# Optimization experiments

Hardware: AMD Instinct MI355X
Metric: run time of the kernel (lower is better)

## Reference

```python
import jax, jax.numpy as jnp
import numpy as np
import math

H, NH, NKV, HD, FF = 1024, 16, 4, 64, 4096
B, S = 2, 2048
EPS, THETA = 1e-6, 10000.0


def _rmsnorm(x, w, eps=EPS):
    v = jnp.mean(x.astype(jnp.float32) ** 2, axis=-1, keepdims=True)
    return (x.astype(jnp.float32) * jax.lax.rsqrt(v + eps)).astype(x.dtype) * w


def _rope_tables(seq_len, head_dim, theta=THETA):
    inv_freq = 1.0 / (theta ** (jnp.arange(0, head_dim, 2, dtype=jnp.float32) / head_dim))
    freqs = jnp.arange(seq_len, dtype=jnp.float32)[:, None] * inv_freq[None, :]
    emb = jnp.concatenate([freqs, freqs], axis=-1)  # [S, HD]
    return jnp.cos(emb), jnp.sin(emb)


def _rotate_half(x):
    x1, x2 = jnp.split(x, 2, axis=-1)
    return jnp.concatenate([-x2, x1], axis=-1)


def _apply_rope(x, cos, sin):
    # x: [B, h, S, HD]; cos/sin: [S, HD] broadcast over batch/heads
    return x * cos[None, None] + _rotate_half(x) * sin[None, None]


def setup_inputs() -> dict:
    key = jax.random.key(0)
    ks = jax.random.split(key, 12)
    std = 0.02
    return {
        "hidden_states": jax.random.normal(ks[0], (B, S, H), jnp.float32),
        "kv_states": jax.random.normal(ks[1], (B, S, H), jnp.float32),
        "attention_mask": jnp.zeros((B, 1, S, S), jnp.float32),
        "ln1_w": jnp.ones((H,), jnp.float32),
        "ln2_w": jnp.ones((H,), jnp.float32),
        "Wq": jax.random.normal(ks[2], (H, NH * HD), jnp.float32) * std,
        "Wk": jax.random.normal(ks[3], (H, NKV * HD), jnp.float32) * std,
        "Wv": jax.random.normal(ks[4], (H, NKV * HD), jnp.float32) * std,
        "Wo": jax.random.normal(ks[5], (NH * HD, H), jnp.float32) * std,
        "Wgate": jax.random.normal(ks[6], (H, FF), jnp.float32) * std,
        "Wup": jax.random.normal(ks[7], (H, FF), jnp.float32) * std,
        "Wdown": jax.random.normal(ks[8], (FF, H), jnp.float32) * std,
    }


def reference(hidden_states, kv_states, attention_mask, ln1_w, ln2_w,
              Wq, Wk, Wv, Wo, Wgate, Wup, Wdown):
    bsz, q_len, _ = hidden_states.shape
    k_len = kv_states.shape[1]

    residual = hidden_states
    h = _rmsnorm(hidden_states, ln1_w)   # input_layernorm on queries
    kv = _rmsnorm(kv_states, ln1_w)      # same norm applied to kv_states

    q = (h @ Wq).reshape(bsz, q_len, NH, HD).transpose(0, 2, 1, 3)    # [B,NH,Sq,HD]
    k = (kv @ Wk).reshape(bsz, k_len, NKV, HD).transpose(0, 2, 1, 3)  # [B,NKV,Sk,HD]
    v = (kv @ Wv).reshape(bsz, k_len, NKV, HD).transpose(0, 2, 1, 3)

    cos_q, sin_q = _rope_tables(q_len, HD)
    cos_k, sin_k = _rope_tables(k_len, HD)
    q = _apply_rope(q, cos_q, sin_q)
    k = _apply_rope(k, cos_k, sin_k)

    # repeat_kv: GQA expand to NH heads
    groups = NH // NKV
    k = jnp.repeat(k, groups, axis=1)
    v = jnp.repeat(v, groups, axis=1)

    scores = jnp.einsum("bhqd,bhkd->bhqk", q, k) / math.sqrt(HD)
    scores = scores + attention_mask  # additive mask [B,1,Sq,Sk]
    probs = jax.nn.softmax(scores.astype(jnp.float32), axis=-1).astype(q.dtype)
    attn = jnp.einsum("bhqk,bhkd->bhqd", probs, v)
    attn = attn.transpose(0, 2, 1, 3).reshape(bsz, q_len, NH * HD)
    attn = attn @ Wo

    hidden = residual + attn

    residual = hidden
    x = _rmsnorm(hidden, ln2_w)
    x = (jax.nn.silu(x @ Wgate) * (x @ Wup)) @ Wdown  # SwiGLU MLP
    return residual + x
```

## Files before the change

kernel.cpp:

```cpp
#include <hip/hip_runtime.h>
#include <math.h>

#define SS 2048

typedef __attribute__((ext_vector_type(8))) short s16x8;
typedef __attribute__((ext_vector_type(4))) float f32x4;
typedef __attribute__((ext_vector_type(16))) float f32x16;

__device__ __forceinline__ unsigned short f2bf(float f) {
  union { float f; unsigned u; } a; a.f = f;
  unsigned r = a.u + 0x7fffu + ((a.u >> 16) & 1u);
  return (unsigned short)(r >> 16);
}
__device__ __forceinline__ float bf2f(unsigned short b) {
  union { unsigned u; float f; } a; a.u = ((unsigned)b) << 16;
  return a.f;
}
__device__ __forceinline__ unsigned cvtpk(float a, float b) {
  unsigned d; asm("v_cvt_pk_bf16_f32 %0, %1, %2" : "=v"(d) : "v"(a), "v"(b)); return d;
}
__device__ __forceinline__ float fexp2(float x) {
  float r; asm("v_exp_f32 %0, %1" : "=v"(r) : "v"(x)); return r;
}
__device__ __forceinline__ void async16(void* lds, const void* g) {
  __builtin_amdgcn_global_load_lds(
      (const __attribute__((address_space(1))) unsigned int*)g,
      (__attribute__((address_space(3))) unsigned int*)lds, 16, 0, 0);
}
__device__ __forceinline__ f32x4 mfma_bf16(s16x8 a, s16x8 b, f32x4 c) {
  return __builtin_amdgcn_mfma_f32_16x16x32_bf16(a, b, c, 0, 0, 0);
}
__device__ __forceinline__ f32x16 mfma32(s16x8 a, s16x8 b, f32x16 c) {
  return __builtin_amdgcn_mfma_f32_32x32x16_bf16(a, b, c, 0, 0, 0);
}

__global__ __launch_bounds__(256) void k_transpose(const float* __restrict__ W,
                                                   unsigned short* __restrict__ WT,
                                                   int K, int N) {
  __shared__ float tile[32][33];
  int t = threadIdx.x;
  int tx = t & 31, ty = t >> 5;
  int n0 = blockIdx.x * 32, k0 = blockIdx.y * 32;
#pragma unroll
  for (int i = 0; i < 4; ++i)
    tile[ty + 8 * i][tx] = W[(size_t)(k0 + ty + 8 * i) * N + n0 + tx];
  __syncthreads();
#pragma unroll
  for (int i = 0; i < 4; ++i)
    WT[(size_t)(n0 + ty + 8 * i) * K + k0 + tx] = f2bf(tile[tx][ty + 8 * i]);
}

__global__ __launch_bounds__(256) void k_vtrans(const unsigned short* __restrict__ QKV,
                                                unsigned short* __restrict__ VT) {
  __shared__ unsigned short tile[32][33];
  int t = threadIdx.x, tx = t & 31, ty = t >> 5;
  int s0 = blockIdx.x * 32, d0 = blockIdx.y * 32;
  int bk = blockIdx.z; int b = bk >> 2, kvh = bk & 3;
#pragma unroll
  for (int i = 0; i < 4; ++i)
    tile[ty + 8 * i][tx] =
        QKV[((size_t)b * SS + s0 + ty + 8 * i) * 1536 + 1280 + kvh * 64 + d0 + tx];
  __syncthreads();
#pragma unroll
  for (int i = 0; i < 4; ++i)
    VT[((size_t)bk * 64 + d0 + ty + 8 * i) * SS + s0 + tx] = tile[tx][ty + 8 * i];
}

__global__ void k_rope_tables(float* __restrict__ cosT, float* __restrict__ sinT) {
  int idx = blockIdx.x * 256 + threadIdx.x;
  int s = idx >> 5, i = idx & 31;
  double ang = (double)s * pow(10000.0, -(double)(2 * i) / 64.0);
  cosT[idx] = (float)cos(ang);
  sinT[idx] = (float)sin(ang);
}

__global__ __launch_bounds__(256) void k_rmsnorm(const float* __restrict__ X,
                                                 const float* __restrict__ Wt,
                                                 unsigned short* __restrict__ Y) {
  int row = blockIdx.x, t = threadIdx.x;
  float4 v = ((const float4*)X)[(size_t)row * 256 + t];
  float ssq = v.x * v.x + v.y * v.y + v.z * v.z + v.w * v.w;
#pragma unroll
  for (int m = 1; m < 64; m <<= 1) ssq += __shfl_xor(ssq, m);
  __shared__ float red[4];
  if ((t & 63) == 0) red[t >> 6] = ssq;
  __syncthreads();
  float sc = rsqrtf((red[0] + red[1] + red[2] + red[3]) * (1.0f / 1024.0f) + 1e-6f);
  float4 wv = ((const float4*)Wt)[t];
  ushort4 o;
  o.x = f2bf(v.x * sc * wv.x); o.y = f2bf(v.y * sc * wv.y);
  o.z = f2bf(v.z * sc * wv.z); o.w = f2bf(v.w * sc * wv.w);
  ((ushort4*)Y)[(size_t)row * 256 + t] = o;
}

__global__ __launch_bounds__(256) void k_rope(unsigned short* __restrict__ X,
                                              const float* __restrict__ cosT,
                                              const float* __restrict__ sinT,
                                              int stride) {
  int idx = blockIdx.x * 256 + threadIdx.x;
  int seg = idx & 7, tok = idx >> 3;
  int head = blockIdx.y;
  int s = tok & (SS - 1);
  int d0 = seg * 4;
  unsigned short* p = X + (size_t)tok * stride + head * 64;
  ushort4 lo = *(ushort4*)&p[d0];
  ushort4 hi = *(ushort4*)&p[d0 + 32];
  float4 cs = *(const float4*)&cosT[s * 32 + d0];
  float4 sn = *(const float4*)&sinT[s * 32 + d0];
  ushort4 olo, ohi;
  olo.x = f2bf(bf2f(lo.x) * cs.x - bf2f(hi.x) * sn.x);
  olo.y = f2bf(bf2f(lo.y) * cs.y - bf2f(hi.y) * sn.y);
  olo.z = f2bf(bf2f(lo.z) * cs.z - bf2f(hi.z) * sn.z);
  olo.w = f2bf(bf2f(lo.w) * cs.w - bf2f(hi.w) * sn.w);
  ohi.x = f2bf(bf2f(hi.x) * cs.x + bf2f(lo.x) * sn.x);
  ohi.y = f2bf(bf2f(hi.y) * cs.y + bf2f(lo.y) * sn.y);
  ohi.z = f2bf(bf2f(hi.z) * cs.z + bf2f(lo.z) * sn.z);
  ohi.w = f2bf(bf2f(hi.w) * cs.w + bf2f(lo.w) * sn.w);
  *(ushort4*)&p[d0] = olo;
  *(ushort4*)&p[d0 + 32] = ohi;
}

template <int EPI, int BN>
__global__ __launch_bounds__(256) void k_gemm(const unsigned short* __restrict__ A,
                                              const unsigned short* __restrict__ BT,
                                              int K, int ldc,
                                              unsigned short* Cb,
                                              float* __restrict__ Cf,
                                              const float* __restrict__ Res) {
  constexpr int NW = BN / 32;
  __shared__ __align__(16) unsigned short at[128 * 32];
  __shared__ __align__(16) unsigned short bt[BN * 32];
  int t = threadIdx.x, w = t >> 6, l = t & 63;
  int g = l >> 4, c = l & 15;
  int wm = w >> 1, wn = w & 1;
  f32x4 acc[4][NW] = {};
  const unsigned short* gA = A + (size_t)(blockIdx.y * 128 + (t >> 2)) * K + (t & 3) * 8;
  const unsigned short* gB = BT + (size_t)(blockIdx.x * BN + (t >> 2)) * K + (t & 3) * 8;
  unsigned short* dA = &at[w * 512];
  unsigned short* dB = &bt[w * 512];
  const int nk = K >> 5;
  for (int kt = 0; kt < nk; ++kt) {
    async16(dA, gA);
    async16(dA + 2048, gA + (size_t)64 * K);
    async16(dB, gB);
    if (BN == 128) async16(dB + 2048, gB + (size_t)64 * K);
    gA += 32; gB += 32;
    __syncthreads();
    s16x8 af[4], bfr[NW];
#pragma unroll
    for (int m = 0; m < 4; ++m) af[m] = *(const s16x8*)&at[(wm * 64 + m * 16 + c) * 32 + g * 8];
#pragma unroll
    for (int n = 0; n < NW; ++n)
      bfr[n] = *(const s16x8*)&bt[(wn * (BN / 2) + n * 16 + c) * 32 + g * 8];
#pragma unroll
    for (int m = 0; m < 4; ++m)
#pragma unroll
      for (int n = 0; n < NW; ++n)
        acc[m][n] = mfma_bf16(af[m], bfr[n], acc[m][n]);
    __syncthreads();
  }
  size_t rb = (size_t)blockIdx.y * 128 + wm * 64;
  size_t cbase = (size_t)blockIdx.x * BN + wn * (BN / 2);
#pragma unroll
  for (int m = 0; m < 4; ++m)
#pragma unroll
    for (int n = 0; n < NW; ++n)
#pragma unroll
      for (int r = 0; r < 4; ++r) {
        size_t row = rb + m * 16 + g * 4 + r;
        size_t col = cbase + n * 16 + c;
        float v = acc[m][n][r];
        if (EPI == 0) Cb[row * ldc + col] = f2bf(v);
        else Cf[row * ldc + col] = v + Res[row * ldc + col];
      }
}

__global__ __launch_bounds__(512) void k_gateup(const unsigned short* __restrict__ A,
                                                const unsigned short* __restrict__ BTg,
                                                const unsigned short* __restrict__ BTu,
                                                unsigned short* __restrict__ Cb) {
  __shared__ __align__(16) unsigned short at[128 * 32];
  __shared__ __align__(16) unsigned short bg[128 * 32];
  __shared__ __align__(16) unsigned short bu[128 * 32];
  int t = threadIdx.x, w = t >> 6, l = t & 63;
  int g = l >> 4, c = l & 15;
  int wm = w >> 2, wn = w & 3;
  f32x4 ag[4][2] = {}, au[4][2] = {};
  const unsigned short* gA = A + (size_t)(blockIdx.y * 128 + (t >> 2)) * 1024 + (t & 3) * 8;
  const unsigned short* gG = BTg + (size_t)(blockIdx.x * 128 + (t >> 2)) * 1024 + (t & 3) * 8;
  const unsigned short* gU = BTu + (size_t)(blockIdx.x * 128 + (t >> 2)) * 1024 + (t & 3) * 8;
  unsigned short* dA = &at[w * 512];
  unsigned short* dG = &bg[w * 512];
  unsigned short* dU = &bu[w * 512];
  for (int kt = 0; kt < 32; ++kt) {
    async16(dA, gA);
    async16(dG, gG);
    async16(dU, gU);
    gA += 32; gG += 32; gU += 32;
    __syncthreads();
    s16x8 af[4], bgf[2], buf_[2];
#pragma unroll
    for (int m = 0; m < 4; ++m) af[m] = *(const s16x8*)&at[(wm * 64 + m * 16 + c) * 32 + g * 8];
#pragma unroll
    for (int n = 0; n < 2; ++n) {
      bgf[n] = *(const s16x8*)&bg[(wn * 32 + n * 16 + c) * 32 + g * 8];
      buf_[n] = *(const s16x8*)&bu[(wn * 32 + n * 16 + c) * 32 + g * 8];
    }
#pragma unroll
    for (int m = 0; m < 4; ++m)
#pragma unroll
      for (int n = 0; n < 2; ++n) {
        ag[m][n] = mfma_bf16(af[m], bgf[n], ag[m][n]);
        au[m][n] = mfma_bf16(af[m], buf_[n], au[m][n]);
      }
    __syncthreads();
  }
  size_t rb = (size_t)blockIdx.y * 128 + wm * 64;
  size_t cb = (size_t)blockIdx.x * 128 + wn * 32;
#pragma unroll
  for (int m = 0; m < 4; ++m)
#pragma unroll
    for (int n = 0; n < 2; ++n)
#pragma unroll
      for (int r = 0; r < 4; ++r) {
        size_t row = rb + m * 16 + g * 4 + r;
        size_t col = cb + n * 16 + c;
        float gv = ag[m][n][r], uv = au[m][n][r];
        Cb[row * 4096 + col] = f2bf(gv / (1.0f + __expf(-gv)) * uv);
      }
}

__global__ __launch_bounds__(256) void k_attn(const unsigned short* __restrict__ Q,
                                              const unsigned short* __restrict__ K,
                                              const unsigned short* __restrict__ VT,
                                              const float* __restrict__ mask,
                                              unsigned short* __restrict__ Out) {
  __shared__ __align__(16) unsigned short Ks[2][64 * 64];
  __shared__ __align__(16) unsigned short VTs[2][64 * 64];
  const float LOG2E = 1.44269504f;
  int t = threadIdx.x, w = t >> 6, l = t & 63;
  int q32 = l & 31, hi = l >> 5;
  int blk = blockIdx.x;
  int qt = blk & 63, kvh = (blk >> 6) & 3, b = blk >> 8;
  int head = kvh * 4 + w;
  size_t tokQ = (size_t)b * SS + qt * 32;

  s16x8 qfr[4];
#pragma unroll
  for (int d = 0; d < 4; ++d)
    qfr[d] = *(const s16x8*)&Q[(tokQ + q32) * 1536 + head * 64 + d * 16 + hi * 8];
  const s16x8 one8 = {(short)0x3F80, (short)0x3F80, (short)0x3F80, (short)0x3F80,
                      (short)0x3F80, (short)0x3F80, (short)0x3F80, (short)0x3F80};

  int id0 = t, id1 = t + 256;
  int row0 = id0 >> 3, b80 = id0 & 7;
  int row1 = id1 >> 3, b81 = id1 & 7;
  int so0 = row0 * 64 + ((b80 ^ (row0 & 7)) << 3);
  int so1 = row1 * 64 + ((b81 ^ (row1 & 7)) << 3);
  const unsigned short* gK = K + (size_t)b * SS * 1536 + kvh * 64;
  const unsigned short* gV = VT + (size_t)(b * 4 + kvh) * 64 * SS;

  int4 rK0 = *(const int4*)(gK + (size_t)row0 * 1536 + b80 * 8);
  int4 rK1 = *(const int4*)(gK + (size_t)row1 * 1536 + b81 * 8);
  int4 rV0 = *(const int4*)(gV + (size_t)row0 * SS + b80 * 8);
  int4 rV1 = *(const int4*)(gV + (size_t)row1 * SS + b81 * 8);
  *(int4*)&Ks[0][so0] = rK0; *(int4*)&Ks[0][so1] = rK1;
  *(int4*)&VTs[0][so0] = rV0; *(int4*)&VTs[0][so1] = rV1;

  const float* mrowp = mask + (size_t)b * SS * SS + (size_t)(qt * 32 + q32) * SS + 4 * hi;
  float mc0[16], mc1[16];
#pragma unroll
  for (int j = 0; j < 4; ++j) {
    float4 v0 = *(const float4*)&mrowp[8 * j];
    float4 v1 = *(const float4*)&mrowp[32 + 8 * j];
    mc0[4 * j] = v0.x; mc0[4 * j + 1] = v0.y; mc0[4 * j + 2] = v0.z; mc0[4 * j + 3] = v0.w;
    mc1[4 * j] = v1.x; mc1[4 * j + 1] = v1.y; mc1[4 * j + 2] = v1.z; mc1[4 * j + 3] = v1.w;
  }

  f32x16 aco0 = {}, aco1 = {}, acl = {};
  float mrun = -1e30f;
  __syncthreads();

  for (int kt = 0; kt < 32; ++kt) {
    const unsigned short* Kc = Ks[kt & 1];
    const unsigned short* Vc = VTs[kt & 1];
    if (kt < 31) {
      int kb = (kt + 1) * 64;
      rK0 = *(const int4*)(gK + (size_t)(kb + row0) * 1536 + b80 * 8);
      rK1 = *(const int4*)(gK + (size_t)(kb + row1) * 1536 + b81 * 8);
      rV0 = *(const int4*)(gV + (size_t)row0 * SS + kb + b80 * 8);
      rV1 = *(const int4*)(gV + (size_t)row1 * SS + kb + b81 * 8);
    }
    f32x16 s0 = {}, s1 = {};
    __builtin_amdgcn_s_setprio(1);
#pragma unroll
    for (int d = 0; d < 4; ++d) {
      s16x8 ka = *(const s16x8*)&Kc[q32 * 64 + (((d * 2 + hi) ^ (q32 & 7)) << 3)];
      s0 = mfma32(ka, qfr[d], s0);
      int r2 = 32 + q32;
      s16x8 kb2 = *(const s16x8*)&Kc[r2 * 64 + (((d * 2 + hi) ^ (r2 & 7)) << 3)];
      s1 = mfma32(kb2, qfr[d], s1);
    }
    __builtin_amdgcn_s_setprio(0);
    float sv0[16], sv1[16];
#pragma unroll
    for (int r = 0; r < 16; ++r) {
      sv0[r] = (s0[r] * 0.125f + mc0[r]) * LOG2E;
      sv1[r] = (s1[r] * 0.125f + mc1[r]) * LOG2E;
    }
    {
      int nk = (kt < 31 ? kt + 1 : 31) * 64;
#pragma unroll
      for (int j = 0; j < 4; ++j) {
        float4 v0 = *(const float4*)&mrowp[nk + 8 * j];
        float4 v1 = *(const float4*)&mrowp[nk + 32 + 8 * j];
        mc0[4 * j] = v0.x; mc0[4 * j + 1] = v0.y; mc0[4 * j + 2] = v0.z; mc0[4 * j + 3] = v0.w;
        mc1[4 * j] = v1.x; mc1[4 * j + 1] = v1.y; mc1[4 * j + 2] = v1.z; mc1[4 * j + 3] = v1.w;
      }
    }
    float mx = sv0[0];
#pragma unroll
    for (int r = 1; r < 16; ++r) mx = fmaxf(mx, sv0[r]);
#pragma unroll
    for (int r = 0; r < 16; ++r) mx = fmaxf(mx, sv1[r]);
    mx = fmaxf(mx, __shfl_xor(mx, 32));
    if (__any(mx > mrun + 8.0f)) {
      float mnew = fmaxf(mrun, mx);
      float alpha = fexp2(mrun - mnew);
      mrun = mnew;
#pragma unroll
      for (int r = 0; r < 16; ++r) {
        float al = __shfl(alpha, (r & 3) + 8 * (r >> 2) + 4 * hi);
        aco0[r] *= al; aco1[r] *= al; acl[r] *= al;
      }
    }
    s16x8 pa[4];
#pragma unroll
    for (int ks = 0; ks < 2; ++ks) {
      float p[16];
      if (ks == 0) {
#pragma unroll
        for (int r = 0; r < 16; ++r) p[r] = fexp2(sv0[r] - mrun);
      } else {
#pragma unroll
        for (int r = 0; r < 16; ++r) p[r] = fexp2(sv1[r] - mrun);
      }
      unsigned w8[8];
#pragma unroll
      for (int i = 0; i < 8; ++i) w8[i] = cvtpk(p[2 * i], p[2 * i + 1]);
      unsigned sd0 = hi ? w8[0] : w8[2];
      unsigned sd1 = hi ? w8[1] : w8[3];
      unsigned sd2 = hi ? w8[4] : w8[6];
      unsigned sd3 = hi ? w8[5] : w8[7];
      unsigned rc0 = (unsigned)__shfl_xor((int)sd0, 32);
      unsigned rc1 = (unsigned)__shfl_xor((int)sd1, 32);
      unsigned rc2 = (unsigned)__shfl_xor((int)sd2, 32);
      unsigned rc3 = (unsigned)__shfl_xor((int)sd3, 32);
      union { int4 i; s16x8 v; } fa, fb;
      fa.i.x = hi ? rc0 : w8[0]; fa.i.y = hi ? rc1 : w8[1];
      fa.i.z = hi ? w8[2] : rc0; fa.i.w = hi ? w8[3] : rc1;
      fb.i.x = hi ? rc2 : w8[4]; fb.i.y = hi ? rc3 : w8[5];
      fb.i.z = hi ? w8[6] : rc2; fb.i.w = hi ? w8[7] : rc3;
      pa[2 * ks] = fa.v;
      pa[2 * ks + 1] = fb.v;
    }
    __builtin_amdgcn_s_setprio(1);
#pragma unroll
    for (int ks = 0; ks < 4; ++ks) {
      s16x8 va = *(const s16x8*)&Vc[q32 * 64 + (((ks * 2 + hi) ^ (q32 & 7)) << 3)];
      aco0 = mfma32(pa[ks], va, aco0);
      int r2 = 32 + q32;
      s16x8 vb2 = *(const s16x8*)&Vc[r2 * 64 + (((ks * 2 + hi) ^ (r2 & 7)) << 3)];
      aco1 = mfma32(pa[ks], vb2, aco1);
      acl = mfma32(pa[ks], one8, acl);
    }
    __builtin_amdgcn_s_setprio(0);
    if (kt < 31) {
      int nb = (kt + 1) & 1;
      *(int4*)&Ks[nb][so0] = rK0; *(int4*)&Ks[nb][so1] = rK1;
      *(int4*)&VTs[nb][so0] = rV0; *(int4*)&VTs[nb][so1] = rV1;
    }
    __syncthreads();
  }
#pragma unroll
  for (int r = 0; r < 16; ++r) {
    float inv = 1.0f / acl[r];
    size_t orow = tokQ + (r & 3) + 8 * (r >> 2) + 4 * hi;
    Out[orow * 1024 + head * 64 + q32] = f2bf(aco0[r] * inv);
    Out[orow * 1024 + head * 64 + 32 + q32] = f2bf(aco1[r] * inv);
  }
}

extern "C" void kernel_launch(void* const* d_in, const int* in_sizes, int n_in,
                              void* d_out, int out_size, void* d_ws, size_t ws_size,
                              hipStream_t stream) {
  (void)in_sizes; (void)n_in; (void)out_size; (void)ws_size;
  const float* hidden = (const float*)d_in[0];
  const float* kvst   = (const float*)d_in[1];
  const float* maskp  = (const float*)d_in[2];
  const float* ln1    = (const float*)d_in[3];
  const float* ln2    = (const float*)d_in[4];
  const float* Wq     = (const float*)d_in[5];
  const float* Wk     = (const float*)d_in[6];
  const float* Wv     = (const float*)d_in[7];
  const float* Wo     = (const float*)d_in[8];
  const float* Wg     = (const float*)d_in[9];
  const float* Wu     = (const float*)d_in[10];
  const float* Wd     = (const float*)d_in[11];
  float* out = (float*)d_out;

  char* ws = (char*)d_ws;
  size_t off = 0;
  auto alloc = [&](size_t bytes) { char* p = ws + off; off += (bytes + 255) & ~(size_t)255; return p; };
  unsigned short* WTqkv = (unsigned short*)alloc((size_t)1536 * 1024 * 2);
  unsigned short* WTo   = (unsigned short*)alloc((size_t)1024 * 1024 * 2);
  unsigned short* WTg   = (unsigned short*)alloc((size_t)4096 * 1024 * 2);
  unsigned short* WTu   = (unsigned short*)alloc((size_t)4096 * 1024 * 2);
  unsigned short* WTd   = (unsigned short*)alloc((size_t)1024 * 4096 * 2);
  float* cosT           = (float*)alloc((size_t)2048 * 32 * 4);
  float* sinT           = (float*)alloc((size_t)2048 * 32 * 4);
  unsigned short* hn    = (unsigned short*)alloc((size_t)4096 * 1024 * 2);
  unsigned short* kvn   = (unsigned short*)alloc((size_t)4096 * 1024 * 2);
  unsigned short* QKVb  = (unsigned short*)alloc((size_t)4096 * 1536 * 2);
  unsigned short* VTg   = (unsigned short*)alloc((size_t)8 * 64 * SS * 2);
  float* hid2           = (float*)alloc((size_t)4096 * 1024 * 4);
  unsigned short* inter = (unsigned short*)alloc((size_t)4096 * 4096 * 2);
  unsigned short* attnb = hn;
  unsigned short* h2n   = kvn;

  k_transpose<<<dim3(32, 32), 256, 0, stream>>>(Wq, WTqkv, 1024, 1024);
  k_transpose<<<dim3(8, 32), 256, 0, stream>>>(Wk, WTqkv + (size_t)1024 * 1024, 1024, 256);
  k_transpose<<<dim3(8, 32), 256, 0, stream>>>(Wv, WTqkv + (size_t)1280 * 1024, 1024, 256);
  k_transpose<<<dim3(32, 32), 256, 0, stream>>>(Wo, WTo, 1024, 1024);
  k_transpose<<<dim3(128, 32), 256, 0, stream>>>(Wg, WTg, 1024, 4096);
  k_transpose<<<dim3(128, 32), 256, 0, stream>>>(Wu, WTu, 1024, 4096);
  k_transpose<<<dim3(32, 128), 256, 0, stream>>>(Wd, WTd, 4096, 1024);
  k_rope_tables<<<256, 256, 0, stream>>>(cosT, sinT);
  k_rmsnorm<<<4096, 256, 0, stream>>>(hidden, ln1, hn);
  k_rmsnorm<<<4096, 256, 0, stream>>>(kvst, ln1, kvn);
  k_gemm<0, 64><<<dim3(16, 32), 256, 0, stream>>>(hn, WTqkv, 1024, 1536, QKVb, nullptr, nullptr);
  k_gemm<0, 64><<<dim3(8, 32), 256, 0, stream>>>(kvn, WTqkv + (size_t)1024 * 1024, 1024, 1536,
                                                 QKVb + 1024, nullptr, nullptr);
  k_rope<<<dim3(128, 20), 256, 0, stream>>>(QKVb, cosT, sinT, 1536);
  k_vtrans<<<dim3(64, 2, 8), 256, 0, stream>>>(QKVb, VTg);
  k_attn<<<512, 256, 0, stream>>>(QKVb, QKVb + 1024, VTg, maskp, attnb);
  k_gemm<1, 64><<<dim3(16, 32), 256, 0, stream>>>(attnb, WTo, 1024, 1024, nullptr, hid2, hidden);
  k_rmsnorm<<<4096, 256, 0, stream>>>(hid2, ln2, h2n);
  k_gateup<<<dim3(32, 32), 512, 0, stream>>>(h2n, WTg, WTu, inter);
  k_gemm<1, 64><<<dim3(16, 32), 256, 0, stream>>>(inter, WTd, 4096, 1024, nullptr, out, hid2);
}
```

Measured before the change: 337.4 us.

## Split attention KV range across two wave groups and merge partial softmax

The attention block grows from 256 to 512 threads. Each of two wave groups handles half of the key/value sequence, with its own double-buffered LDS tiles. At the end, group 1 writes its partial numerators, denominators and running max to LDS. Group 0 then rescales and merges them flash-decoding style before writing the output. This doubles the waves per CU and halves the serial KV loop, at the cost of 64KB of LDS per block and an extra merge step.

```diff
diff --git a/kernel.cpp b/kernel.cpp
--- a/kernel.cpp
+++ b/kernel.cpp
@@ -230,20 +230,23 @@
       }
 }
 
-__global__ __launch_bounds__(256) void k_attn(const unsigned short* __restrict__ Q,
+__global__ __launch_bounds__(512) void k_attn(const unsigned short* __restrict__ Q,
                                               const unsigned short* __restrict__ K,
                                               const unsigned short* __restrict__ VT,
                                               const float* __restrict__ mask,
                                               unsigned short* __restrict__ Out) {
-  __shared__ __align__(16) unsigned short Ks[2][64 * 64];
-  __shared__ __align__(16) unsigned short VTs[2][64 * 64];
+  __shared__ __align__(16) char smem[65536];
   const float LOG2E = 1.44269504f;
   int t = threadIdx.x, w = t >> 6, l = t & 63;
   int q32 = l & 31, hi = l >> 5;
+  int th = w >> 2, hh = w & 3;
   int blk = blockIdx.x;
   int qt = blk & 63, kvh = (blk >> 6) & 3, b = blk >> 8;
-  int head = kvh * 4 + w;
+  int head = kvh * 4 + hh;
   size_t tokQ = (size_t)b * SS + qt * 32;
+
+  unsigned short* KsT = (unsigned short*)(smem + th * 32768);
+  unsigned short* VTsT = (unsigned short*)(smem + th * 32768 + 16384);
 
   s16x8 qfr[4];
 #pragma unroll
@@ -252,22 +255,24 @@
   const s16x8 one8 = {(short)0x3F80, (short)0x3F80, (short)0x3F80, (short)0x3F80,
                       (short)0x3F80, (short)0x3F80, (short)0x3F80, (short)0x3F80};
 
-  int id0 = t, id1 = t + 256;
+  int tt = t & 255;
+  int id0 = tt, id1 = tt + 256;
   int row0 = id0 >> 3, b80 = id0 & 7;
   int row1 = id1 >> 3, b81 = id1 & 7;
   int so0 = row0 * 64 + ((b80 ^ (row0 & 7)) << 3);
   int so1 = row1 * 64 + ((b81 ^ (row1 & 7)) << 3);
   const unsigned short* gK = K + (size_t)b * SS * 1536 + kvh * 64;
   const unsigned short* gV = VT + (size_t)(b * 4 + kvh) * 64 * SS;
-
-  int4 rK0 = *(const int4*)(gK + (size_t)row0 * 1536 + b80 * 8);
-  int4 rK1 = *(const int4*)(gK + (size_t)row1 * 1536 + b81 * 8);
-  int4 rV0 = *(const int4*)(gV + (size_t)row0 * SS + b80 * 8);
-  int4 rV1 = *(const int4*)(gV + (size_t)row1 * SS + b81 * 8);
-  *(int4*)&Ks[0][so0] = rK0; *(int4*)&Ks[0][so1] = rK1;
-  *(int4*)&VTs[0][so0] = rV0; *(int4*)&VTs[0][so1] = rV1;
-
-  const float* mrowp = mask + (size_t)b * SS * SS + (size_t)(qt * 32 + q32) * SS + 4 * hi;
+  const int tb = th * 1024;
+
+  int4 rK0 = *(const int4*)(gK + (size_t)(tb + row0) * 1536 + b80 * 8);
+  int4 rK1 = *(const int4*)(gK + (size_t)(tb + row1) * 1536 + b81 * 8);
+  int4 rV0 = *(const int4*)(gV + (size_t)row0 * SS + tb + b80 * 8);
+  int4 rV1 = *(const int4*)(gV + (size_t)row1 * SS + tb + b81 * 8);
+  *(int4*)&KsT[so0] = rK0; *(int4*)&KsT[so1] = rK1;
+  *(int4*)&VTsT[so0] = rV0; *(int4*)&VTsT[so1] = rV1;
+
+  const float* mrowp = mask + (size_t)b * SS * SS + (size_t)(qt * 32 + q32) * SS + 4 * hi + tb;
   float mc0[16], mc1[16];
 #pragma unroll
   for (int j = 0; j < 4; ++j) {
@@ -281,11 +286,11 @@
   float mrun = -1e30f;
   __syncthreads();
 
-  for (int kt = 0; kt < 32; ++kt) {
-    const unsigned short* Kc = Ks[kt & 1];
-    const unsigned short* Vc = VTs[kt & 1];
-    if (kt < 31) {
-      int kb = (kt + 1) * 64;
+  for (int kt = 0; kt < 16; ++kt) {
+    const unsigned short* Kc = &KsT[(kt & 1) * 4096];
+    const unsigned short* Vc = &VTsT[(kt & 1) * 4096];
+    if (kt < 15) {
+      int kb = tb + (kt + 1) * 64;
       rK0 = *(const int4*)(gK + (size_t)(kb + row0) * 1536 + b80 * 8);
       rK1 = *(const int4*)(gK + (size_t)(kb + row1) * 1536 + b81 * 8);
       rV0 = *(const int4*)(gV + (size_t)row0 * SS + kb + b80 * 8);
@@ -309,7 +314,7 @@
       sv1[r] = (s1[r] * 0.125f + mc1[r]) * LOG2E;
     }
     {
-      int nk = (kt < 31 ? kt + 1 : 31) * 64;
+      int nk = (kt < 15 ? kt + 1 : 15) * 64;
 #pragma unroll
       for (int j = 0; j < 4; ++j) {
         float4 v0 = *(const float4*)&mrowp[nk + 8 * j];
@@ -375,19 +380,37 @@
       acl = mfma32(pa[ks], one8, acl);
     }
     __builtin_amdgcn_s_setprio(0);
-    if (kt < 31) {
+    if (kt < 15) {
       int nb = (kt + 1) & 1;
-      *(int4*)&Ks[nb][so0] = rK0; *(int4*)&Ks[nb][so1] = rK1;
-      *(int4*)&VTs[nb][so0] = rV0; *(int4*)&VTs[nb][so1] = rV1;
+      *(int4*)&KsT[nb * 4096 + so0] = rK0; *(int4*)&KsT[nb * 4096 + so1] = rK1;
+      *(int4*)&VTsT[nb * 4096 + so0] = rV0; *(int4*)&VTsT[nb * 4096 + so1] = rV1;
     }
     __syncthreads();
   }
-#pragma unroll
-  for (int r = 0; r < 16; ++r) {
-    float inv = 1.0f / acl[r];
-    size_t orow = tokQ + (r & 3) + 8 * (r >> 2) + 4 * hi;
-    Out[orow * 1024 + head * 64 + q32] = f2bf(aco0[r] * inv);
-    Out[orow * 1024 + head * 64 + 32 + q32] = f2bf(aco1[r] * inv);
+
+  float* exch = (float*)smem;
+  float* e = &exch[(hh * 64 + l) * 49];
+  if (th == 1) {
+#pragma unroll
+    for (int r = 0; r < 16; ++r) { e[r] = aco0[r]; e[16 + r] = aco1[r]; e[32 + r] = acl[r]; }
+    e[48] = mrun;
+  }
+  __syncthreads();
+  if (th == 0) {
+    float m1 = e[48];
+    float M = fmaxf(mrun, m1);
+    float a0 = fexp2(mrun - M), a1 = fexp2(m1 - M);
+#pragma unroll
+    for (int r = 0; r < 16; ++r) {
+      int src = (r & 3) + 8 * (r >> 2) + 4 * hi;
+      float al0 = __shfl(a0, src), al1 = __shfl(a1, src);
+      float num0 = aco0[r] * al0 + e[r] * al1;
+      float num1 = aco1[r] * al0 + e[16 + r] * al1;
+      float inv = 1.0f / (acl[r] * al0 + e[32 + r] * al1);
+      size_t orow = tokQ + src;
+      Out[orow * 1024 + head * 64 + q32] = f2bf(num0 * inv);
+      Out[orow * 1024 + head * 64 + 32 + q32] = f2bf(num1 * inv);
+    }
   }
 }
 
@@ -443,7 +466,7 @@
                                                  QKVb + 1024, nullptr, nullptr);
   k_rope<<<dim3(128, 20), 256, 0, stream>>>(QKVb, cosT, sinT, 1536);
   k_vtrans<<<dim3(64, 2, 8), 256, 0, stream>>>(QKVb, VTg);
-  k_attn<<<512, 256, 0, stream>>>(QKVb, QKVb + 1024, VTg, maskp, attnb);
+  k_attn<<<512, 512, 0, stream>>>(QKVb, QKVb + 1024, VTg, maskp, attnb);
   k_gemm<1, 64><<<dim3(16, 32), 256, 0, stream>>>(attnb, WTo, 1024, 1024, nullptr, hid2, hidden);
   k_rmsnorm<<<4096, 256, 0, stream>>>(hid2, ln2, h2n);
   k_gateup<<<dim3(32, 32), 512, 0, stream>>>(h2n, WTg, WTu, inter);
```

New measurement: 342.8 us. No clear change (+1.6%).

## Split attention over two KV halves and merge partials in a combine kernel

Applied to the files above, without the earlier changes.

The attention kernel now splits the key sequence into two halves, doubling the grid from 512 to 1024 blocks. Each block writes unnormalised fp32 partial outputs plus its running max and row sum, and a new combine kernel rescales and merges the two halves into the bf16 output. The goal is better occupancy across the GPU's compute units, since 512 blocks may underfill the device. In exchange it adds an extra launch, fp32 partial traffic of about 32 MB written and read back, and reuse of workspace buffers for the partials.

```diff
diff --git a/kernel.cpp b/kernel.cpp
--- a/kernel.cpp
+++ b/kernel.cpp
@@ -234,16 +234,19 @@
                                               const unsigned short* __restrict__ K,
                                               const unsigned short* __restrict__ VT,
                                               const float* __restrict__ mask,
-                                              unsigned short* __restrict__ Out) {
+                                              float* __restrict__ Opart,
+                                              float* __restrict__ Mpart,
+                                              float* __restrict__ Lpart) {
   __shared__ __align__(16) unsigned short Ks[2][64 * 64];
   __shared__ __align__(16) unsigned short VTs[2][64 * 64];
   const float LOG2E = 1.44269504f;
   int t = threadIdx.x, w = t >> 6, l = t & 63;
   int q32 = l & 31, hi = l >> 5;
   int blk = blockIdx.x;
-  int qt = blk & 63, kvh = (blk >> 6) & 3, b = blk >> 8;
+  int half = blk & 1, qt = (blk >> 1) & 63, kvh = (blk >> 7) & 3, b = blk >> 9;
   int head = kvh * 4 + w;
   size_t tokQ = (size_t)b * SS + qt * 32;
+  const int tb = half * 1024;
 
   s16x8 qfr[4];
 #pragma unroll
@@ -260,14 +263,14 @@
   const unsigned short* gK = K + (size_t)b * SS * 1536 + kvh * 64;
   const unsigned short* gV = VT + (size_t)(b * 4 + kvh) * 64 * SS;
 
-  int4 rK0 = *(const int4*)(gK + (size_t)row0 * 1536 + b80 * 8);
-  int4 rK1 = *(const int4*)(gK + (size_t)row1 * 1536 + b81 * 8);
-  int4 rV0 = *(const int4*)(gV + (size_t)row0 * SS + b80 * 8);
-  int4 rV1 = *(const int4*)(gV + (size_t)row1 * SS + b81 * 8);
+  int4 rK0 = *(const int4*)(gK + (size_t)(tb + row0) * 1536 + b80 * 8);
+  int4 rK1 = *(const int4*)(gK + (size_t)(tb + row1) * 1536 + b81 * 8);
+  int4 rV0 = *(const int4*)(gV + (size_t)row0 * SS + tb + b80 * 8);
+  int4 rV1 = *(const int4*)(gV + (size_t)row1 * SS + tb + b81 * 8);
   *(int4*)&Ks[0][so0] = rK0; *(int4*)&Ks[0][so1] = rK1;
   *(int4*)&VTs[0][so0] = rV0; *(int4*)&VTs[0][so1] = rV1;
 
-  const float* mrowp = mask + (size_t)b * SS * SS + (size_t)(qt * 32 + q32) * SS + 4 * hi;
+  const float* mrowp = mask + (size_t)b * SS * SS + (size_t)(qt * 32 + q32) * SS + 4 * hi + tb;
   float mc0[16], mc1[16];
 #pragma unroll
   for (int j = 0; j < 4; ++j) {
@@ -281,11 +284,11 @@
   float mrun = -1e30f;
   __syncthreads();
 
-  for (int kt = 0; kt < 32; ++kt) {
+  for (int kt = 0; kt < 16; ++kt) {
     const unsigned short* Kc = Ks[kt & 1];
     const unsigned short* Vc = VTs[kt & 1];
-    if (kt < 31) {
-      int kb = (kt + 1) * 64;
+    if (kt < 15) {
+      int kb = tb + (kt + 1) * 64;
       rK0 = *(const int4*)(gK + (size_t)(kb + row0) * 1536 + b80 * 8);
       rK1 = *(const int4*)(gK + (size_t)(kb + row1) * 1536 + b81 * 8);
       rV0 = *(const int4*)(gV + (size_t)row0 * SS + kb + b80 * 8);
@@ -309,7 +312,7 @@
       sv1[r] = (s1[r] * 0.125f + mc1[r]) * LOG2E;
     }
     {
-      int nk = (kt < 31 ? kt + 1 : 31) * 64;
+      int nk = (kt < 15 ? kt + 1 : 15) * 64;
 #pragma unroll
       for (int j = 0; j < 4; ++j) {
         float4 v0 = *(const float4*)&mrowp[nk + 8 * j];
@@ -375,20 +378,49 @@
       acl = mfma32(pa[ks], one8, acl);
     }
     __builtin_amdgcn_s_setprio(0);
-    if (kt < 31) {
+    if (kt < 15) {
       int nb = (kt + 1) & 1;
       *(int4*)&Ks[nb][so0] = rK0; *(int4*)&Ks[nb][so1] = rK1;
       *(int4*)&VTs[nb][so0] = rV0; *(int4*)&VTs[nb][so1] = rV1;
     }
     __syncthreads();
   }
+  size_t pbase = (size_t)half * 4096 + tokQ;
 #pragma unroll
   for (int r = 0; r < 16; ++r) {
-    float inv = 1.0f / acl[r];
-    size_t orow = tokQ + (r & 3) + 8 * (r >> 2) + 4 * hi;
-    Out[orow * 1024 + head * 64 + q32] = f2bf(aco0[r] * inv);
-    Out[orow * 1024 + head * 64 + 32 + q32] = f2bf(aco1[r] * inv);
+    size_t orow = pbase + (r & 3) + 8 * (r >> 2) + 4 * hi;
+    Opart[orow * 1024 + head * 64 + q32] = aco0[r];
+    Opart[orow * 1024 + head * 64 + 32 + q32] = aco1[r];
   }
+  if (hi == 0)
+    Mpart[(pbase + q32) * 16 + head] = mrun;
+  if (q32 == 0)
+#pragma unroll
+    for (int r = 0; r < 16; ++r)
+      Lpart[(pbase + (r & 3) + 8 * (r >> 2) + 4 * hi) * 16 + head] = acl[r];
+}
+
+__global__ __launch_bounds__(256) void k_comb(const float* __restrict__ Opart,
+                                              const float* __restrict__ Mpart,
+                                              const float* __restrict__ Lpart,
+                                              unsigned short* __restrict__ Out) {
+  int tok = blockIdx.x, t = threadIdx.x;
+  int col = t * 4, head = col >> 6;
+  float m0 = Mpart[(size_t)tok * 16 + head];
+  float m1 = Mpart[(size_t)(4096 + tok) * 16 + head];
+  float l0 = Lpart[(size_t)tok * 16 + head];
+  float l1 = Lpart[(size_t)(4096 + tok) * 16 + head];
+  float M = fmaxf(m0, m1);
+  float a0 = fexp2(m0 - M), a1 = fexp2(m1 - M);
+  float inv = 1.0f / (l0 * a0 + l1 * a1);
+  float4 O0 = *(const float4*)&Opart[(size_t)tok * 1024 + col];
+  float4 O1 = *(const float4*)&Opart[(size_t)(4096 + tok) * 1024 + col];
+  ushort4 o;
+  o.x = f2bf((O0.x * a0 + O1.x * a1) * inv);
+  o.y = f2bf((O0.y * a0 + O1.y * a1) * inv);
+  o.z = f2bf((O0.z * a0 + O1.z * a1) * inv);
+  o.w = f2bf((O0.w * a0 + O1.w * a1) * inv);
+  *(ushort4*)&Out[(size_t)tok * 1024 + col] = o;
 }
 
 extern "C" void kernel_launch(void* const* d_in, const int* in_sizes, int n_in,
@@ -427,6 +459,9 @@
   unsigned short* inter = (unsigned short*)alloc((size_t)4096 * 4096 * 2);
   unsigned short* attnb = hn;
   unsigned short* h2n   = kvn;
+  float* Opart          = (float*)inter;
+  float* Mpart          = hid2;
+  float* Lpart          = hid2 + 8192 * 16;
 
   k_transpose<<<dim3(32, 32), 256, 0, stream>>>(Wq, WTqkv, 1024, 1024);
   k_transpose<<<dim3(8, 32), 256, 0, stream>>>(Wk, WTqkv + (size_t)1024 * 1024, 1024, 256);
@@ -443,7 +478,8 @@
                                                  QKVb + 1024, nullptr, nullptr);
   k_rope<<<dim3(128, 20), 256, 0, stream>>>(QKVb, cosT, sinT, 1536);
   k_vtrans<<<dim3(64, 2, 8), 256, 0, stream>>>(QKVb, VTg);
-  k_attn<<<512, 256, 0, stream>>>(QKVb, QKVb + 1024, VTg, maskp, attnb);
+  k_attn<<<1024, 256, 0, stream>>>(QKVb, QKVb + 1024, VTg, maskp, Opart, Mpart, Lpart);
+  k_comb<<<4096, 256, 0, stream>>>(Opart, Mpart, Lpart, attnb);
   k_gemm<1, 64><<<dim3(16, 32), 256, 0, stream>>>(attnb, WTo, 1024, 1024, nullptr, hid2, hidden);
   k_rmsnorm<<<4096, 256, 0, stream>>>(hid2, ln2, h2n);
   k_gateup<<<dim3(32, 32), 512, 0, stream>>>(h2n, WTg, WTu, inter);
```

After: 377.6 us. 11.9% more time.

## Swizzle GEMM blocks across XCDs and prefetch attention mask two tiles ahead

Applied to the files above, without the earlier changes.

Adds an XCD-aware block index remap to the generic GEMM and gate/up kernels, so blocks that share A/B tiles land on the same chiplet's L2. In attention, the mask tile is now double-buffered in registers and loaded two key tiles ahead, which gives the global load more time to complete before it is used. The register pressure in the attention kernel rises by 32 floats per thread. The swizzle assumes the workgroup count divides evenly by 8.

```diff
diff --git a/kernel.cpp b/kernel.cpp
--- a/kernel.cpp
+++ b/kernel.cpp
@@ -32,6 +32,13 @@
 }
 __device__ __forceinline__ f32x16 mfma32(s16x8 a, s16x8 b, f32x16 c) {
   return __builtin_amdgcn_mfma_f32_32x32x16_bf16(a, b, c, 0, 0, 0);
+}
+__device__ __forceinline__ void xcd_swz(int& bx, int& by) {
+  int nx = gridDim.x;
+  int nwg = nx * gridDim.y;
+  int bid = blockIdx.y * nx + blockIdx.x;
+  int sid = (bid & 7) * (nwg >> 3) + (bid >> 3);
+  bx = sid % nx; by = sid / nx;
 }
 
 __global__ __launch_bounds__(256) void k_transpose(const float* __restrict__ W,
@@ -130,12 +137,13 @@
   constexpr int NW = BN / 32;
   __shared__ __align__(16) unsigned short at[128 * 32];
   __shared__ __align__(16) unsigned short bt[BN * 32];
+  int bx, by; xcd_swz(bx, by);
   int t = threadIdx.x, w = t >> 6, l = t & 63;
   int g = l >> 4, c = l & 15;
   int wm = w >> 1, wn = w & 1;
   f32x4 acc[4][NW] = {};
-  const unsigned short* gA = A + (size_t)(blockIdx.y * 128 + (t >> 2)) * K + (t & 3) * 8;
-  const unsigned short* gB = BT + (size_t)(blockIdx.x * BN + (t >> 2)) * K + (t & 3) * 8;
+  const unsigned short* gA = A + (size_t)(by * 128 + (t >> 2)) * K + (t & 3) * 8;
+  const unsigned short* gB = BT + (size_t)(bx * BN + (t >> 2)) * K + (t & 3) * 8;
   unsigned short* dA = &at[w * 512];
   unsigned short* dB = &bt[w * 512];
   const int nk = K >> 5;
@@ -159,8 +167,8 @@
         acc[m][n] = mfma_bf16(af[m], bfr[n], acc[m][n]);
     __syncthreads();
   }
-  size_t rb = (size_t)blockIdx.y * 128 + wm * 64;
-  size_t cbase = (size_t)blockIdx.x * BN + wn * (BN / 2);
+  size_t rb = (size_t)by * 128 + wm * 64;
+  size_t cbase = (size_t)bx * BN + wn * (BN / 2);
 #pragma unroll
   for (int m = 0; m < 4; ++m)
 #pragma unroll
@@ -182,13 +190,14 @@
   __shared__ __align__(16) unsigned short at[128 * 32];
   __shared__ __align__(16) unsigned short bg[128 * 32];
   __shared__ __align__(16) unsigned short bu[128 * 32];
+  int bx, by; xcd_swz(bx, by);
   int t = threadIdx.x, w = t >> 6, l = t & 63;
   int g = l >> 4, c = l & 15;
   int wm = w >> 2, wn = w & 3;
   f32x4 ag[4][2] = {}, au[4][2] = {};
-  const unsigned short* gA = A + (size_t)(blockIdx.y * 128 + (t >> 2)) * 1024 + (t & 3) * 8;
-  const unsigned short* gG = BTg + (size_t)(blockIdx.x * 128 + (t >> 2)) * 1024 + (t & 3) * 8;
-  const unsigned short* gU = BTu + (size_t)(blockIdx.x * 128 + (t >> 2)) * 1024 + (t & 3) * 8;
+  const unsigned short* gA = A + (size_t)(by * 128 + (t >> 2)) * 1024 + (t & 3) * 8;
+  const unsigned short* gG = BTg + (size_t)(bx * 128 + (t >> 2)) * 1024 + (t & 3) * 8;
+  const unsigned short* gU = BTu + (size_t)(bx * 128 + (t >> 2)) * 1024 + (t & 3) * 8;
   unsigned short* dA = &at[w * 512];
   unsigned short* dG = &bg[w * 512];
   unsigned short* dU = &bu[w * 512];
@@ -215,8 +224,8 @@
       }
     __syncthreads();
   }
-  size_t rb = (size_t)blockIdx.y * 128 + wm * 64;
-  size_t cb = (size_t)blockIdx.x * 128 + wn * 32;
+  size_t rb = (size_t)by * 128 + wm * 64;
+  size_t cb = (size_t)bx * 128 + wn * 32;
 #pragma unroll
   for (int m = 0; m < 4; ++m)
 #pragma unroll
@@ -268,20 +277,25 @@
   *(int4*)&VTs[0][so0] = rV0; *(int4*)&VTs[0][so1] = rV1;
 
   const float* mrowp = mask + (size_t)b * SS * SS + (size_t)(qt * 32 + q32) * SS + 4 * hi;
-  float mc0[16], mc1[16];
-#pragma unroll
-  for (int j = 0; j < 4; ++j) {
-    float4 v0 = *(const float4*)&mrowp[8 * j];
-    float4 v1 = *(const float4*)&mrowp[32 + 8 * j];
-    mc0[4 * j] = v0.x; mc0[4 * j + 1] = v0.y; mc0[4 * j + 2] = v0.z; mc0[4 * j + 3] = v0.w;
-    mc1[4 * j] = v1.x; mc1[4 * j + 1] = v1.y; mc1[4 * j + 2] = v1.z; mc1[4 * j + 3] = v1.w;
-  }
+  float mA0[16], mA1[16], mB0[16], mB1[16];
+  auto LDM = [&](float (&m0)[16], float (&m1)[16], int nk) {
+#pragma unroll
+    for (int j = 0; j < 4; ++j) {
+      float4 v0 = *(const float4*)&mrowp[nk + 8 * j];
+      float4 v1 = *(const float4*)&mrowp[nk + 32 + 8 * j];
+      m0[4 * j] = v0.x; m0[4 * j + 1] = v0.y; m0[4 * j + 2] = v0.z; m0[4 * j + 3] = v0.w;
+      m1[4 * j] = v1.x; m1[4 * j + 1] = v1.y; m1[4 * j + 2] = v1.z; m1[4 * j + 3] = v1.w;
+    }
+  };
+  LDM(mA0, mA1, 0);
+  LDM(mB0, mB1, 64);
 
   f32x16 aco0 = {}, aco1 = {}, acl = {};
   float mrun = -1e30f;
   __syncthreads();
 
-  for (int kt = 0; kt < 32; ++kt) {
+  auto STEP = [&](int kt, float (&mc0)[16], float (&mc1)[16],
+                  float (&mp0)[16], float (&mp1)[16]) {
     const unsigned short* Kc = Ks[kt & 1];
     const unsigned short* Vc = VTs[kt & 1];
     if (kt < 31) {
@@ -309,14 +323,8 @@
       sv1[r] = (s1[r] * 0.125f + mc1[r]) * LOG2E;
     }
     {
-      int nk = (kt < 31 ? kt + 1 : 31) * 64;
-#pragma unroll
-      for (int j = 0; j < 4; ++j) {
-        float4 v0 = *(const float4*)&mrowp[nk + 8 * j];
-        float4 v1 = *(const float4*)&mrowp[nk + 32 + 8 * j];
-        mc0[4 * j] = v0.x; mc0[4 * j + 1] = v0.y; mc0[4 * j + 2] = v0.z; mc0[4 * j + 3] = v0.w;
-        mc1[4 * j] = v1.x; mc1[4 * j + 1] = v1.y; mc1[4 * j + 2] = v1.z; mc1[4 * j + 3] = v1.w;
-      }
+      int nk = (kt + 2 <= 31 ? kt + 2 : 31) * 64;
+      LDM(mp0, mp1, nk);
     }
     float mx = sv0[0];
 #pragma unroll
@@ -381,6 +389,11 @@
       *(int4*)&VTs[nb][so0] = rV0; *(int4*)&VTs[nb][so1] = rV1;
     }
     __syncthreads();
+  };
+
+  for (int kt2 = 0; kt2 < 32; kt2 += 2) {
+    STEP(kt2, mA0, mA1, mA0, mA1);
+    STEP(kt2 + 1, mB0, mB1, mB0, mB1);
   }
 #pragma unroll
   for (int r = 0; r < 16; ++r) {
```

After: 370.5 us. 9.8% more time.
